# Kernel optimization log

Hardware: AMD Instinct MI355X
Metric: run time of the kernel (lower is better)

Reference implementation:

```python
import jax, jax.numpy as jnp
import numpy as np

HIDDEN = 256
HEADS = 8
HEAD_DIM = HIDDEN // HEADS


def setup_inputs() -> dict:
    key = jax.random.key(0)
    ks = jax.random.split(key, 8)
    B, N, L, C = 8, 512, 24, HIDDEN
    s = 1.0 / np.sqrt(C)
    return {
        "spatial_nodes": jax.random.normal(ks[0], (B, N, C), jnp.float32),
        "temporal_nodes": jax.random.normal(ks[1], (B, N, L, C), jnp.float32),
        "Wq": jax.random.normal(ks[2], (C, C), jnp.float32) * s,
        "bq": jnp.zeros((C,), jnp.float32),
        "Wkv": jax.random.normal(ks[3], (C, 2 * C), jnp.float32) * s,
        "bkv": jnp.zeros((2 * C,), jnp.float32),
        "Wo": jax.random.normal(ks[4], (C, C), jnp.float32) * s,
        "bo": jnp.zeros((C,), jnp.float32),
    }


def reference(spatial_nodes, temporal_nodes, Wq, bq, Wkv, bkv, Wo, bo):
    B, N, C = spatial_nodes.shape
    L = temporal_nodes.shape[2]
    H, D = HEADS, HEAD_DIM
    q = spatial_nodes @ Wq + bq                      # [B,N,C]
    kv = temporal_nodes @ Wkv + bkv                  # [B,N,L,2C]
    k, v = jnp.split(kv, 2, axis=-1)                 # each [B,N,L,C]
    q = q.reshape(B, N, H, D)
    k = k.reshape(B, N, L, H, D)
    v = v.reshape(B, N, L, H, D)
    scores = jnp.einsum('bnhd,bnlhd->bnhl', q, k) / jnp.sqrt(jnp.float32(D))
    attn = jax.nn.softmax(scores, axis=-1)           # dropout is identity in eval
    out = jnp.einsum('bnhl,bnlhd->bnhd', attn, v).reshape(B, N, C)
    return out @ Wo + bo
```

## Files before the change

kernel.cpp:

```cpp
#include <hip/hip_runtime.h>
#include <hip/hip_bf16.h>


#define L_ 24
#define C_ 256
#define H_ 8
#define D_ 32
#define NTOK 4096
#define SCALE 0.17677669529663687f

typedef __attribute__((ext_vector_type(8))) short short8;
typedef __attribute__((ext_vector_type(4))) float f32x4;

#define QK_OFF   ((size_t)0)
#define TBAR_OFF ((size_t)16777216)
#define MT_OFF   ((size_t)33554432)
#define W2T_OFF  ((size_t)34603008)
#define BQK_OFF  ((size_t)35651584)
#define BO2_OFF  ((size_t)35659776)
#define WS_NEED  ((size_t)35660800)

__global__ __launch_bounds__(256)
void k_pre(const float* __restrict__ Wq, const float* __restrict__ bq,
           const float* __restrict__ Wkv, const float* __restrict__ bkv,
           const float* __restrict__ Wo, const float* __restrict__ bo,
           char* __restrict__ ws)
{
    __hip_bfloat16* mt  = (__hip_bfloat16*)(ws + MT_OFF);
    __hip_bfloat16* w2t = (__hip_bfloat16*)(ws + W2T_OFF);
    float* bqk = (float*)(ws + BQK_OFF);
    float* bo2 = (float*)(ws + BO2_OFF);
    const int b = blockIdx.x, tid = threadIdx.x;
    __shared__ float sW[32][33];
    if (b < 128) {
        const bool isV = b >= 64;
        const int bb = isV ? b - 64 : b;
        const int h = bb >> 3, c0 = (bb & 7) * 32;
        {
            const int ci = tid >> 3, dq = (tid & 7) * 4;
            const float4 v = *(const float4*)(Wkv + (size_t)(c0 + ci) * 512 + (isV ? 256 : 0) + h * 32 + dq);
            sW[ci][dq + 0] = v.x; sW[ci][dq + 1] = v.y; sW[ci][dq + 2] = v.z; sW[ci][dq + 3] = v.w;
        }
        __syncthreads();
        const int e = tid;
        float wreg[32];
        if (!isV) {
#pragma unroll
            for (int dq = 0; dq < 32; dq += 4) {
                const float4 v = *(const float4*)(Wq + (size_t)e * 256 + h * 32 + dq);
                wreg[dq] = v.x; wreg[dq + 1] = v.y; wreg[dq + 2] = v.z; wreg[dq + 3] = v.w;
            }
            for (int ci = 0; ci < 32; ++ci) {
                float a = 0.f;
#pragma unroll
                for (int d = 0; d < 32; ++d) a = fmaf(wreg[d], sW[ci][d], a);
                mt[(size_t)(h * 256 + c0 + ci) * 256 + e] = __float2bfloat16(a * SCALE);
            }
        } else {
#pragma unroll
            for (int d = 0; d < 32; ++d) wreg[d] = Wo[(size_t)(h * 32 + d) * 256 + e];
            __hip_bfloat16 accs[32];
            for (int ci = 0; ci < 32; ++ci) {
                float a = 0.f;
#pragma unroll
                for (int d = 0; d < 32; ++d) a = fmaf(wreg[d], sW[ci][d], a);
                accs[ci] = __float2bfloat16(a);
            }
#pragma unroll
            for (int g = 0; g < 4; ++g)
                *(uint4*)&w2t[(size_t)e * 2048 + h * 256 + c0 + g * 8] = *(const uint4*)&accs[g * 8];
        }
    } else if (b == 128) {
        const int c = tid;
        const float* row = Wkv + (size_t)c * 512;
#pragma unroll
        for (int h = 0; h < 8; ++h) {
            float a = 0.f;
#pragma unroll
            for (int dq = 0; dq < 32; dq += 4) {
                const float4 v = *(const float4*)(row + h * 32 + dq);
                a = fmaf(bq[h * 32 + dq + 0], v.x, a);
                a = fmaf(bq[h * 32 + dq + 1], v.y, a);
                a = fmaf(bq[h * 32 + dq + 2], v.z, a);
                a = fmaf(bq[h * 32 + dq + 3], v.w, a);
            }
            bqk[h * 256 + c] = a * SCALE;
        }
    } else {
        const int e = tid;
        float a = bo[e];
        for (int hd = 0; hd < 256; ++hd)
            a = fmaf(bkv[256 + hd], Wo[(size_t)hd * 256 + e], a);
        bo2[e] = a;
    }
}

__global__ __launch_bounds__(256)
void k_qk(const float* __restrict__ S, char* __restrict__ ws)
{
    const __hip_bfloat16* mt = (const __hip_bfloat16*)(ws + MT_OFF);
    const float* bqk = (const float*)(ws + BQK_OFF);
    __hip_bfloat16* qk = (__hip_bfloat16*)(ws + QK_OFF);
    __shared__ __hip_bfloat16 sA[64][72];
    __shared__ __hip_bfloat16 sB[64][72];
    const int tid = threadIdx.x;
    const int bm = blockIdx.x & 63, bn = blockIdx.x >> 6;
    const int m0 = bm * 64, n0 = bn * 64;
    const int w = tid >> 6, L = tid & 63;
    const int wr = (w >> 1) * 32, wc = (w & 1) * 32;
    const int fr = L & 15, fk = (L >> 4) * 8;
    const int sr = tid >> 2, sc = (tid & 3) * 16;
    f32x4 acc[2][2] = {};
    for (int k0 = 0; k0 < 256; k0 += 64) {
        {
            const float* p = S + (size_t)(m0 + sr) * 256 + k0 + sc;
            union { __hip_bfloat16 h[16]; uint4 u[2]; } pk;
#pragma unroll
            for (int q = 0; q < 4; ++q) {
                const float4 v = *(const float4*)(p + q * 4);
                pk.h[q * 4 + 0] = __float2bfloat16(v.x);
                pk.h[q * 4 + 1] = __float2bfloat16(v.y);
                pk.h[q * 4 + 2] = __float2bfloat16(v.z);
                pk.h[q * 4 + 3] = __float2bfloat16(v.w);
            }
            *(uint4*)&sA[sr][sc]     = pk.u[0];
            *(uint4*)&sA[sr][sc + 8] = pk.u[1];
            const uint4* pb = (const uint4*)(mt + (size_t)(n0 + sr) * 256 + k0 + sc);
            *(uint4*)&sB[sr][sc]     = pb[0];
            *(uint4*)&sB[sr][sc + 8] = pb[1];
        }
        __syncthreads();
#pragma unroll
        for (int kh = 0; kh < 2; ++kh) {
            const int fk2 = kh * 32 + fk;
            const short8 af0 = *(const short8*)&sA[wr +  0 + fr][fk2];
            const short8 af1 = *(const short8*)&sA[wr + 16 + fr][fk2];
            const short8 bf0 = *(const short8*)&sB[wc +  0 + fr][fk2];
            const short8 bf1 = *(const short8*)&sB[wc + 16 + fr][fk2];
            acc[0][0] = __builtin_amdgcn_mfma_f32_16x16x32_bf16(af0, bf0, acc[0][0], 0, 0, 0);
            acc[0][1] = __builtin_amdgcn_mfma_f32_16x16x32_bf16(af0, bf1, acc[0][1], 0, 0, 0);
            acc[1][0] = __builtin_amdgcn_mfma_f32_16x16x32_bf16(af1, bf0, acc[1][0], 0, 0, 0);
            acc[1][1] = __builtin_amdgcn_mfma_f32_16x16x32_bf16(af1, bf1, acc[1][1], 0, 0, 0);
        }
        __syncthreads();
    }
#pragma unroll
    for (int i = 0; i < 2; ++i)
#pragma unroll
    for (int j = 0; j < 2; ++j) {
        const int col = n0 + wc + j * 16 + fr;
        const float bb = bqk[col];
#pragma unroll
        for (int r = 0; r < 4; ++r) {
            const int row = m0 + wr + i * 16 + (L >> 4) * 4 + r;
            qk[(size_t)row * 2048 + col] = __float2bfloat16(acc[i][j][r] + bb);
        }
    }
}

__global__ __launch_bounds__(256)
void k_attn(const float* __restrict__ T, char* __restrict__ ws)
{
    const __hip_bfloat16* qk = (const __hip_bfloat16*)(ws + QK_OFF);
    __hip_bfloat16* tbar = (__hip_bfloat16*)(ws + TBAR_OFF);
    __shared__ __hip_bfloat16   sTb[32][264];
    __shared__ __hip_bfloat16   sqk[16][264];
    __shared__ float            sAt[8][33];
    const int tid = threadIdx.x;
    const int t = blockIdx.x;
    {
        const float4* Tv = (const float4*)(T + (size_t)t * 6144);
#pragma unroll
        for (int k = 0; k < 6; ++k) {
            const int f = tid + k * 256;
            const float4 v = Tv[f];
            const int l = f >> 6, c = (f & 63) * 4;
            __hip_bfloat16 b4[4] = { __float2bfloat16(v.x), __float2bfloat16(v.y),
                                     __float2bfloat16(v.z), __float2bfloat16(v.w) };
            *(uint2*)&sTb[l][c] = *(const uint2*)b4;
        }
    }
    {
        const int h = tid >> 5, c = (tid & 31) * 8;
        *(uint4*)&sqk[h][c] = *(const uint4*)(qk + (size_t)t * 2048 + tid * 8);
    }
    {
        const uint4 z = {0u, 0u, 0u, 0u};
        char* zq = (char*)&sqk[8][0];
        char* zt = (char*)&sTb[24][0];
        *(uint4*)(zq + tid * 16) = z;
        *(uint4*)(zt + tid * 16) = z;
        if (tid < 8) {
            *(uint4*)(zq + 4096 + tid * 16) = z;
            *(uint4*)(zt + 4096 + tid * 16) = z;
        }
    }
    __syncthreads();
    if (tid < 64) {
        const int fr = tid & 15, fk = (tid >> 4) * 8;
        f32x4 acc[2] = {};
#pragma unroll
        for (int ks = 0; ks < 8; ++ks) {
            const short8 a  = *(const short8*)&sqk[fr][ks * 32 + fk];
            const short8 b0 = *(const short8*)&sTb[fr][ks * 32 + fk];
            const short8 b1 = *(const short8*)&sTb[16 + fr][ks * 32 + fk];
            acc[0] = __builtin_amdgcn_mfma_f32_16x16x32_bf16(a, b0, acc[0], 0, 0, 0);
            acc[1] = __builtin_amdgcn_mfma_f32_16x16x32_bf16(a, b1, acc[1], 0, 0, 0);
        }
        if (tid < 32) {
            const int hb = (tid >> 4) * 4, l0 = tid & 15;
#pragma unroll
            for (int r = 0; r < 4; ++r) {
                sAt[hb + r][l0] = acc[0][r];
                if (l0 < 8) sAt[hb + r][16 + l0] = acc[1][r];
            }
        }
    }
    __syncthreads();
    if (tid < 8) {
        float mx = -1e30f;
#pragma unroll
        for (int l = 0; l < 24; ++l) mx = fmaxf(mx, sAt[tid][l]);
        float e[24]; float sum = 0.f;
#pragma unroll
        for (int l = 0; l < 24; ++l) { e[l] = __expf(sAt[tid][l] - mx); sum += e[l]; }
        const float inv = 1.0f / sum;
#pragma unroll
        for (int l = 0; l < 24; ++l) sAt[tid][l] = e[l] * inv;
    }
    __syncthreads();
    {
        const int h = tid >> 5, c0 = (tid & 31) * 8;
        float acc[8] = {};
        for (int l = 0; l < 24; ++l) {
            const float a = sAt[h][l];
            const uint4 v = *(const uint4*)&sTb[l][c0];
            const unsigned int* pu = (const unsigned int*)&v;
#pragma unroll
            for (int j = 0; j < 4; ++j) {
                acc[2 * j]     = fmaf(a, __uint_as_float(pu[j] << 16),          acc[2 * j]);
                acc[2 * j + 1] = fmaf(a, __uint_as_float(pu[j] & 0xffff0000u), acc[2 * j + 1]);
            }
        }
        union { __hip_bfloat16 h8[8]; uint4 u; } pk;
#pragma unroll
        for (int j = 0; j < 8; ++j) pk.h8[j] = __float2bfloat16(acc[j]);
        *(uint4*)&tbar[(size_t)t * 2048 + tid * 8] = pk.u;
    }
}

__global__ __launch_bounds__(256)
void k_out(const char* __restrict__ ws, float* __restrict__ Out)
{
    const __hip_bfloat16* tbar = (const __hip_bfloat16*)(ws + TBAR_OFF);
    const __hip_bfloat16* w2t  = (const __hip_bfloat16*)(ws + W2T_OFF);
    const float* bo2 = (const float*)(ws + BO2_OFF);
    __shared__ __hip_bfloat16 sA[64][136];
    __shared__ __hip_bfloat16 sB[32][136];
    const int tid = threadIdx.x;
    const int bm = blockIdx.x & 63, bn = blockIdx.x >> 6;
    const int m0 = bm * 64, n0 = bn * 32;
    const int w = tid >> 6, L = tid & 63;
    const int fr = L & 15, fkb = (L >> 4) * 8;
    const int ar = tid >> 2, ac = (tid & 3) * 32;
    const int br = tid >> 3, bc = (tid & 7) * 16;
    f32x4 acc[2] = {};
    for (int k0 = 0; k0 < 2048; k0 += 128) {
        {
            const uint4* pa = (const uint4*)(tbar + (size_t)(m0 + ar) * 2048 + k0 + ac);
#pragma unroll
            for (int q = 0; q < 4; ++q)
                *(uint4*)&sA[ar][ac + q * 8] = pa[q];
            const uint4* pb = (const uint4*)(w2t + (size_t)(n0 + br) * 2048 + k0 + bc);
            *(uint4*)&sB[br][bc]     = pb[0];
            *(uint4*)&sB[br][bc + 8] = pb[1];
        }
        __syncthreads();
#pragma unroll
        for (int sub = 0; sub < 4; ++sub) {
            const int kb = sub * 32 + fkb;
            const short8 af = *(const short8*)&sA[w * 16 + fr][kb];
            const short8 b0 = *(const short8*)&sB[ 0 + fr][kb];
            const short8 b1 = *(const short8*)&sB[16 + fr][kb];
            acc[0] = __builtin_amdgcn_mfma_f32_16x16x32_bf16(af, b0, acc[0], 0, 0, 0);
            acc[1] = __builtin_amdgcn_mfma_f32_16x16x32_bf16(af, b1, acc[1], 0, 0, 0);
        }
        __syncthreads();
    }
#pragma unroll
    for (int j = 0; j < 2; ++j) {
        const int col = n0 + j * 16 + fr;
        const float bb = bo2[col];
#pragma unroll
        for (int r = 0; r < 4; ++r) {
            const int row = m0 + w * 16 + (L >> 4) * 4 + r;
            Out[(size_t)row * 256 + col] = acc[j][r] + bb;
        }
    }
}

#define NT    16
#define NTHR  512
#define NBLK  256
#define TSTR  (C_ + 4)
#define QKSTR (C_ + 8)
#define QSTR  (D_ + 4)
#define WKROW 268

__global__ __launch_bounds__(NTHR)
void t2s_attn_fused(const float* __restrict__ S, const float* __restrict__ T,
                    const float* __restrict__ Wq, const float* __restrict__ bq,
                    const float* __restrict__ Wkv, const float* __restrict__ bkv,
                    const float* __restrict__ Wo, const float* __restrict__ bo,
                    float* __restrict__ Out)
{
    __shared__ float            sQ[NT][H_][QSTR];
    __shared__ float            sWk[16 * WKROW];
    __shared__ float            sT[2][L_][TSTR];
    __shared__ __hip_bfloat16   sQKT[NT][H_][QKSTR];
    __shared__ float            sSc[H_][L_ + 8];
    const int tid = threadIdx.x;
    const int g0  = blockIdx.x * NT;
    float4 tp0, tp1, tp2;
    {
        const float* tb = T + (size_t)g0 * (L_ * C_);
        tp0 = *(const float4*)(tb + 0 * 2048 + tid * 4);
        tp1 = *(const float4*)(tb + 1 * 2048 + tid * 4);
        tp2 = *(const float4*)(tb + 2 * 2048 + tid * 4);
    }
    {
        const int col = tid & 255;
        const int t0  = (tid >> 8) * 8;
        float acc[8];
        const float bqv = bq[col];
#pragma unroll
        for (int j = 0; j < 8; ++j) acc[j] = bqv;
        const float* sp = S + (size_t)(g0 + t0) * C_;
        for (int c = 0; c < C_; ++c) {
            const float w = Wq[c * C_ + col];
#pragma unroll
            for (int j = 0; j < 8; ++j)
                acc[j] = fmaf(sp[j * C_ + c], w, acc[j]);
        }
#pragma unroll
        for (int j = 0; j < 8; ++j)
            sQ[t0 + j][col >> 5][col & 31] = acc[j];
    }
    {
        const int e = tid * 4;
        *(float4*)&sT[0][(e >> 8) +  0][e & 255] = tp0;
        *(float4*)&sT[0][(e >> 8) +  8][e & 255] = tp1;
        *(float4*)&sT[0][(e >> 8) + 16][e & 255] = tp2;
    }
    __syncthreads();
    {
        const int cq = tid & 3;
        const int h  = (tid >> 2) & 7;
        const int t  = tid >> 5;
        for (int ct = 0; ct < 16; ++ct) {
            {
                const int hd  = tid & 255, ci2 = tid >> 8;
                const float* wsrc = Wkv + (size_t)(ct * 16) * 512;
#pragma unroll
                for (int j = 0; j < 8; ++j) {
                    const int ci = ci2 + j * 2;
                    sWk[ci * WKROW + (hd >> 5) * 33 + (hd & 31)] = wsrc[(size_t)ci * 512 + hd];
                }
            }
            __syncthreads();
            float a0 = 0.f, a1 = 0.f, a2 = 0.f, a3 = 0.f;
            const float* qrow = &sQ[t][h][0];
            const float* wb   = &sWk[(cq * 4) * WKROW + h * 33];
#pragma unroll
            for (int d = 0; d < D_; ++d) {
                const float qv = qrow[d];
                a0 = fmaf(qv, wb[0 * WKROW + d], a0);
                a1 = fmaf(qv, wb[1 * WKROW + d], a1);
                a2 = fmaf(qv, wb[2 * WKROW + d], a2);
                a3 = fmaf(qv, wb[3 * WKROW + d], a3);
            }
            const int c0 = ct * 16 + cq * 4;
            sQKT[t][h][c0 + 0] = __float2bfloat16(a0);
            sQKT[t][h][c0 + 1] = __float2bfloat16(a1);
            sQKT[t][h][c0 + 2] = __float2bfloat16(a2);
            sQKT[t][h][c0 + 3] = __float2bfloat16(a3);
            __syncthreads();
        }
    }
    const int lane = tid & 63, wav = tid >> 6;
    for (int t = 0; t < NT; ++t) {
        const int cur = t & 1;
        const bool pf = (t + 1 < NT);
        if (pf) {
            const float* tb = T + (size_t)(g0 + t + 1) * (L_ * C_);
            tp0 = *(const float4*)(tb + 0 * 2048 + tid * 4);
            tp1 = *(const float4*)(tb + 1 * 2048 + tid * 4);
            tp2 = *(const float4*)(tb + 2 * 2048 + tid * 4);
        }
        if (tid < 192) {
            const int h = tid / 24, l = tid - h * 24;
            const float* trow = &sT[cur][l][0];
            const unsigned short* qkr = (const unsigned short*)&sQKT[t][h][0];
            float a0 = 0.f, a1 = 0.f, a2 = 0.f, a3 = 0.f;
            for (int c = 0; c < C_; c += 4) {
                const float4 tv = *(const float4*)(trow + c);
                const uint2  qu = *(const uint2*)(qkr + c);
                a0 = fmaf(tv.x, __uint_as_float(qu.x << 16),          a0);
                a1 = fmaf(tv.y, __uint_as_float(qu.x & 0xffff0000u), a1);
                a2 = fmaf(tv.z, __uint_as_float(qu.y << 16),          a2);
                a3 = fmaf(tv.w, __uint_as_float(qu.y & 0xffff0000u), a3);
            }
            sSc[h][l] = (a0 + a1 + a2 + a3) * 0.17677669529663687f;
        }
        __syncthreads();
        if (tid < 8) {
            float mx = -1e30f;
#pragma unroll
            for (int l = 0; l < L_; ++l) mx = fmaxf(mx, sSc[tid][l]);
            float e[L_]; float sum = 0.f;
#pragma unroll
            for (int l = 0; l < L_; ++l) { e[l] = __expf(sSc[tid][l] - mx); sum += e[l]; }
            const float inv = 1.0f / sum;
#pragma unroll
            for (int l = 0; l < L_; ++l) sSc[tid][l] = e[l] * inv;
        }
        __syncthreads();
        {
            const int h = wav, c0 = lane * 4;
            float ax = 0.f, ay = 0.f, az = 0.f, aw = 0.f;
            const float* at = &sSc[h][0];
#pragma unroll
            for (int l = 0; l < L_; ++l) {
                const float  a  = at[l];
                const float4 tv = *(const float4*)&sT[cur][l][c0];
                ax = fmaf(a, tv.x, ax); ay = fmaf(a, tv.y, ay);
                az = fmaf(a, tv.z, az); aw = fmaf(a, tv.w, aw);
            }
            sQKT[t][h][c0 + 0] = __float2bfloat16(ax);
            sQKT[t][h][c0 + 1] = __float2bfloat16(ay);
            sQKT[t][h][c0 + 2] = __float2bfloat16(az);
            sQKT[t][h][c0 + 3] = __float2bfloat16(aw);
        }
        if (pf) {
            const int e = tid * 4;
            *(float4*)&sT[cur ^ 1][(e >> 8) +  0][e & 255] = tp0;
            *(float4*)&sT[cur ^ 1][(e >> 8) +  8][e & 255] = tp1;
            *(float4*)&sT[cur ^ 1][(e >> 8) + 16][e & 255] = tp2;
        }
        __syncthreads();
    }
    {
        const int hd = tid & 255;
        const int h  = hd >> 5;
        const int t0 = (tid >> 8) * 8;
        float acc[8];
        const float bv = bkv[C_ + hd];
#pragma unroll
        for (int j = 0; j < 8; ++j) acc[j] = bv;
        const float* wv = Wkv + C_ + hd;
        for (int c = 0; c < C_; c += 2) {
            const float w0 = wv[(size_t)c * 512];
            const float w1 = wv[(size_t)(c + 1) * 512];
#pragma unroll
            for (int j = 0; j < 8; ++j) {
                const unsigned int u = *(const unsigned int*)&sQKT[t0 + j][h][c];
                acc[j] = fmaf(__uint_as_float(u << 16),          w0, acc[j]);
                acc[j] = fmaf(__uint_as_float(u & 0xffff0000u), w1, acc[j]);
            }
        }
#pragma unroll
        for (int j = 0; j < 8; ++j)
            sQ[t0 + j][h][hd & 31] = acc[j];
    }
    __syncthreads();
    {
        const int col = tid & 255;
        const int t0  = (tid >> 8) * 8;
        float acc[8];
        const float bov = bo[col];
#pragma unroll
        for (int j = 0; j < 8; ++j) acc[j] = bov;
        for (int hd = 0; hd < C_; ++hd) {
            const float w  = Wo[hd * C_ + col];
            const int  hh = hd >> 5, dd = hd & 31;
#pragma unroll
            for (int j = 0; j < 8; ++j)
                acc[j] = fmaf(sQ[t0 + j][hh][dd], w, acc[j]);
        }
#pragma unroll
        for (int j = 0; j < 8; ++j)
            Out[(size_t)(g0 + t0 + j) * C_ + col] = acc[j];
    }
}

extern "C" void kernel_launch(void* const* d_in, const int* in_sizes, int n_in,
                              void* d_out, int out_size, void* d_ws, size_t ws_size,
                              hipStream_t stream) {
    const float* S   = (const float*)d_in[0];
    const float* T   = (const float*)d_in[1];
    const float* Wq  = (const float*)d_in[2];
    const float* bq  = (const float*)d_in[3];
    const float* Wkv = (const float*)d_in[4];
    const float* bkv = (const float*)d_in[5];
    const float* Wo  = (const float*)d_in[6];
    const float* bo  = (const float*)d_in[7];
    float* Out = (float*)d_out;
    if (ws_size >= WS_NEED) {
        char* ws = (char*)d_ws;
        hipLaunchKernelGGL(k_pre,  dim3(130),  dim3(256), 0, stream, Wq, bq, Wkv, bkv, Wo, bo, ws);
        hipLaunchKernelGGL(k_qk,   dim3(2048), dim3(256), 0, stream, S, ws);
        hipLaunchKernelGGL(k_attn, dim3(4096), dim3(256), 0, stream, T, ws);
        hipLaunchKernelGGL(k_out,  dim3(512),  dim3(256), 0, stream, ws, Out);
    } else {
        hipLaunchKernelGGL(t2s_attn_fused, dim3(NBLK), dim3(NTHR), 0, stream,
                           S, T, Wq, bq, Wkv, bkv, Wo, bo, Out);
    }
}
```

Before: 71.44 us.

## Enlarge QK GEMM tile to 128x64 and read qk directly in attention

The QK projection kernel now computes 128x64 output tiles, so each wave holds a 4x2 grid of MFMA accumulators and the grid shrinks from 2048 to 1024 blocks. The aim is more reuse of each B fragment and less redundant loading per output. The attention kernel no longer stages qk rows in shared memory or zero-fills padding rows. MFMA A-fragments are loaded straight from global memory, which removes LDS traffic and shared-memory use. Rows past the token's 8 heads now read neighbouring workspace data, but those results are never used.

Measured after the change: 86.18 us. 20.6% more time.

```diff
diff --git a/kernel.cpp b/kernel.cpp
--- a/kernel.cpp
+++ b/kernel.cpp
@@ -101,51 +101,54 @@
     const __hip_bfloat16* mt = (const __hip_bfloat16*)(ws + MT_OFF);
     const float* bqk = (const float*)(ws + BQK_OFF);
     __hip_bfloat16* qk = (__hip_bfloat16*)(ws + QK_OFF);
-    __shared__ __hip_bfloat16 sA[64][72];
+    __shared__ __hip_bfloat16 sA[128][72];
     __shared__ __hip_bfloat16 sB[64][72];
     const int tid = threadIdx.x;
-    const int bm = blockIdx.x & 63, bn = blockIdx.x >> 6;
-    const int m0 = bm * 64, n0 = bn * 64;
+    const int bm = blockIdx.x & 31, bn = blockIdx.x >> 5;
+    const int m0 = bm * 128, n0 = bn * 64;
     const int w = tid >> 6, L = tid & 63;
-    const int wr = (w >> 1) * 32, wc = (w & 1) * 32;
+    const int wr = (w >> 1) * 64, wc = (w & 1) * 32;
     const int fr = L & 15, fk = (L >> 4) * 8;
-    const int sr = tid >> 2, sc = (tid & 3) * 16;
-    f32x4 acc[2][2] = {};
+    const int asr = tid >> 1, asc = (tid & 1) * 32;
+    const int bsr = tid >> 2, bsc = (tid & 3) * 16;
+    f32x4 acc[4][2] = {};
     for (int k0 = 0; k0 < 256; k0 += 64) {
         {
-            const float* p = S + (size_t)(m0 + sr) * 256 + k0 + sc;
-            union { __hip_bfloat16 h[16]; uint4 u[2]; } pk;
-#pragma unroll
-            for (int q = 0; q < 4; ++q) {
-                const float4 v = *(const float4*)(p + q * 4);
-                pk.h[q * 4 + 0] = __float2bfloat16(v.x);
-                pk.h[q * 4 + 1] = __float2bfloat16(v.y);
-                pk.h[q * 4 + 2] = __float2bfloat16(v.z);
-                pk.h[q * 4 + 3] = __float2bfloat16(v.w);
-            }
-            *(uint4*)&sA[sr][sc]     = pk.u[0];
-            *(uint4*)&sA[sr][sc + 8] = pk.u[1];
-            const uint4* pb = (const uint4*)(mt + (size_t)(n0 + sr) * 256 + k0 + sc);
-            *(uint4*)&sB[sr][sc]     = pb[0];
-            *(uint4*)&sB[sr][sc + 8] = pb[1];
+            const float* p = S + (size_t)(m0 + asr) * 256 + k0 + asc;
+#pragma unroll
+            for (int g = 0; g < 4; ++g) {
+                const float4 v0 = *(const float4*)(p + g * 8);
+                const float4 v1 = *(const float4*)(p + g * 8 + 4);
+                union { __hip_bfloat16 h[8]; uint4 u; } pk;
+                pk.h[0] = __float2bfloat16(v0.x); pk.h[1] = __float2bfloat16(v0.y);
+                pk.h[2] = __float2bfloat16(v0.z); pk.h[3] = __float2bfloat16(v0.w);
+                pk.h[4] = __float2bfloat16(v1.x); pk.h[5] = __float2bfloat16(v1.y);
+                pk.h[6] = __float2bfloat16(v1.z); pk.h[7] = __float2bfloat16(v1.w);
+                *(uint4*)&sA[asr][asc + g * 8] = pk.u;
+            }
+            const uint4* pb = (const uint4*)(mt + (size_t)(n0 + bsr) * 256 + k0 + bsc);
+            *(uint4*)&sB[bsr][bsc]     = pb[0];
+            *(uint4*)&sB[bsr][bsc + 8] = pb[1];
         }
         __syncthreads();
 #pragma unroll
         for (int kh = 0; kh < 2; ++kh) {
-            const int fk2 = kh * 32 + fk;
-            const short8 af0 = *(const short8*)&sA[wr +  0 + fr][fk2];
-            const short8 af1 = *(const short8*)&sA[wr + 16 + fr][fk2];
-            const short8 bf0 = *(const short8*)&sB[wc +  0 + fr][fk2];
-            const short8 bf1 = *(const short8*)&sB[wc + 16 + fr][fk2];
-            acc[0][0] = __builtin_amdgcn_mfma_f32_16x16x32_bf16(af0, bf0, acc[0][0], 0, 0, 0);
-            acc[0][1] = __builtin_amdgcn_mfma_f32_16x16x32_bf16(af0, bf1, acc[0][1], 0, 0, 0);
-            acc[1][0] = __builtin_amdgcn_mfma_f32_16x16x32_bf16(af1, bf0, acc[1][0], 0, 0, 0);
-            acc[1][1] = __builtin_amdgcn_mfma_f32_16x16x32_bf16(af1, bf1, acc[1][1], 0, 0, 0);
-        }
-        __syncthreads();
-    }
-#pragma unroll
-    for (int i = 0; i < 2; ++i)
+            const int f = kh * 32 + fk;
+            short8 af[4], bf[2];
+#pragma unroll
+            for (int i = 0; i < 4; ++i) af[i] = *(const short8*)&sA[wr + i * 16 + fr][f];
+#pragma unroll
+            for (int j = 0; j < 2; ++j) bf[j] = *(const short8*)&sB[wc + j * 16 + fr][f];
+#pragma unroll
+            for (int i = 0; i < 4; ++i)
+#pragma unroll
+            for (int j = 0; j < 2; ++j)
+                acc[i][j] = __builtin_amdgcn_mfma_f32_16x16x32_bf16(af[i], bf[j], acc[i][j], 0, 0, 0);
+        }
+        __syncthreads();
+    }
+#pragma unroll
+    for (int i = 0; i < 4; ++i)
 #pragma unroll
     for (int j = 0; j < 2; ++j) {
         const int col = n0 + wc + j * 16 + fr;
@@ -164,7 +167,6 @@
     const __hip_bfloat16* qk = (const __hip_bfloat16*)(ws + QK_OFF);
     __hip_bfloat16* tbar = (__hip_bfloat16*)(ws + TBAR_OFF);
     __shared__ __hip_bfloat16   sTb[32][264];
-    __shared__ __hip_bfloat16   sqk[16][264];
     __shared__ float            sAt[8][33];
     const int tid = threadIdx.x;
     const int t = blockIdx.x;
@@ -180,28 +182,14 @@
             *(uint2*)&sTb[l][c] = *(const uint2*)b4;
         }
     }
-    {
-        const int h = tid >> 5, c = (tid & 31) * 8;
-        *(uint4*)&sqk[h][c] = *(const uint4*)(qk + (size_t)t * 2048 + tid * 8);
-    }
-    {
-        const uint4 z = {0u, 0u, 0u, 0u};
-        char* zq = (char*)&sqk[8][0];
-        char* zt = (char*)&sTb[24][0];
-        *(uint4*)(zq + tid * 16) = z;
-        *(uint4*)(zt + tid * 16) = z;
-        if (tid < 8) {
-            *(uint4*)(zq + 4096 + tid * 16) = z;
-            *(uint4*)(zt + 4096 + tid * 16) = z;
-        }
-    }
     __syncthreads();
     if (tid < 64) {
         const int fr = tid & 15, fk = (tid >> 4) * 8;
+        const __hip_bfloat16* qrow = qk + (size_t)t * 2048 + fr * 256 + fk;
         f32x4 acc[2] = {};
 #pragma unroll
         for (int ks = 0; ks < 8; ++ks) {
-            const short8 a  = *(const short8*)&sqk[fr][ks * 32 + fk];
+            const short8 a  = *(const short8*)(qrow + ks * 32);
             const short8 b0 = *(const short8*)&sTb[fr][ks * 32 + fk];
             const short8 b1 = *(const short8*)&sTb[16 + fr][ks * 32 + fk];
             acc[0] = __builtin_amdgcn_mfma_f32_16x16x32_bf16(a, b0, acc[0], 0, 0, 0);
@@ -508,7 +496,7 @@
     if (ws_size >= WS_NEED) {
         char* ws = (char*)d_ws;
         hipLaunchKernelGGL(k_pre,  dim3(130),  dim3(256), 0, stream, Wq, bq, Wkv, bkv, Wo, bo, ws);
-        hipLaunchKernelGGL(k_qk,   dim3(2048), dim3(256), 0, stream, S, ws);
+        hipLaunchKernelGGL(k_qk,   dim3(1024), dim3(256), 0, stream, S, ws);
         hipLaunchKernelGGL(k_attn, dim3(4096), dim3(256), 0, stream, T, ws);
         hipLaunchKernelGGL(k_out,  dim3(512),  dim3(256), 0, stream, ws, Out);
     } else {
```
